# Kernel tuning notes

Measured on AMD Instinct MI355X. Metric: run time of the kernel, lower is better.

## Reference

```python
import jax, jax.numpy as jnp
import numpy as np

N = 10000      # nodes
E = 100000     # edges
D = 64         # node_out_feats
EH = 128       # edge_hidden_feats
NI = 74        # node_in_feats
EI = 12        # edge_in_feats
STEPS = 6


def _lin_init(key, fan_in, fan_out):
    s = 1.0 / np.sqrt(fan_in)
    kw, kb = jax.random.split(key)
    W = jax.random.uniform(kw, (fan_out, fan_in), minval=-s, maxval=s, dtype=jnp.float32)
    b = jax.random.uniform(kb, (fan_out,), minval=-s, maxval=s, dtype=jnp.float32)
    return W, b


def setup_inputs() -> dict:
    key = jax.random.key(0)
    ks = jax.random.split(key, 10)
    x = jax.random.normal(ks[0], (N, NI), dtype=jnp.float32)
    edge_index = jax.random.randint(ks[1], (2, E), 0, N, dtype=jnp.int64)
    edge_attr = jax.random.normal(ks[2], (E, EI), dtype=jnp.float32)
    W_proj, b_proj = _lin_init(ks[3], NI, D)
    W_e1, b_e1 = _lin_init(ks[4], EI, EH)
    W_e2, b_e2 = _lin_init(ks[5], EH, D * D)
    W_lin, b_lin = _lin_init(ks[6], D, D)
    s = 1.0 / np.sqrt(D)
    W_ih = jax.random.uniform(ks[7], (3 * D, D), minval=-s, maxval=s, dtype=jnp.float32)
    W_hh = jax.random.uniform(ks[8], (3 * D, D), minval=-s, maxval=s, dtype=jnp.float32)
    kb1, kb2 = jax.random.split(ks[9])
    b_ih = jax.random.uniform(kb1, (3 * D,), minval=-s, maxval=s, dtype=jnp.float32)
    b_hh = jax.random.uniform(kb2, (3 * D,), minval=-s, maxval=s, dtype=jnp.float32)
    return {"x": x, "edge_index": edge_index, "edge_attr": edge_attr,
            "W_proj": W_proj, "b_proj": b_proj,
            "W_e1": W_e1, "b_e1": b_e1, "W_e2": W_e2, "b_e2": b_e2,
            "W_lin": W_lin, "b_lin": b_lin,
            "W_ih": W_ih, "W_hh": W_hh, "b_ih": b_ih, "b_hh": b_hh}


def _gru_cell(x, h, W_ih, W_hh, b_ih, b_hh):
    # torch GRU gate layout: rows [r; z; n]
    gi = x @ W_ih.T + b_ih
    gh = h @ W_hh.T + b_hh
    i_r, i_z, i_n = jnp.split(gi, 3, axis=-1)
    h_r, h_z, h_n = jnp.split(gh, 3, axis=-1)
    r = jax.nn.sigmoid(i_r + h_r)
    z = jax.nn.sigmoid(i_z + h_z)
    n = jnp.tanh(i_n + r * h_n)
    return (1.0 - z) * n + z * h


def reference(x, edge_index, edge_attr, W_proj, b_proj, W_e1, b_e1, W_e2, b_e2,
              W_lin, b_lin, W_ih, W_hh, b_ih, b_hh):
    src = edge_index[0]
    dst = edge_index[1]
    n_nodes = x.shape[0]
    d = W_lin.shape[0]

    # project_node_feats
    node_feats = jax.nn.relu(x @ W_proj.T + b_proj)          # [N, D]
    hidden = node_feats                                       # h0 (never updated, per source)

    # edge network (identical each step in original; compute once)
    eh = jax.nn.relu(edge_attr @ W_e1.T + b_e1)               # [E, EH]
    A = (eh @ W_e2.T + b_e2).reshape(-1, d, d)                # [E, D, D]

    cnt = jax.ops.segment_sum(jnp.ones(src.shape, x.dtype), dst, num_segments=n_nodes)
    cnt = jnp.maximum(cnt, 1.0)[:, None]                      # mean divisor, 0-deg -> keep 0

    for _ in range(STEPS):
        xp = node_feats @ W_lin.T + b_lin                     # lin_node, [N, D]
        msg = jnp.einsum('ed,edf->ef', xp[src], A)            # per-edge bmm, [E, D]
        agg = jax.ops.segment_sum(msg, dst, num_segments=n_nodes) / cnt  # scatter-mean
        nf = jax.nn.relu(agg)
        node_feats = _gru_cell(nf, hidden, W_ih, W_hh, b_ih, b_hh)
    return node_feats
```

## Files before the change

kernel.cpp:

```cpp
#include <hip/hip_runtime.h>
#include <hip/hip_bf16.h>

#define NN 10000
#define NE 100000
#define DD 64
#define EH_ 128
#define NI_ 74
#define EI_ 12
#define NSTEPS 6
#define PADN 10240
#define GCAP 16384
#define EPB 64

#define RZ_OFF 0
#define NI_OFF 16384
#define NH_OFF 20480
#define WL_OFF 24576
#define BE_OFF 28672
#define G_TOT  32768

typedef short bf16x8 __attribute__((ext_vector_type(8)));
typedef float f32x4 __attribute__((ext_vector_type(4)));

static __device__ __forceinline__ unsigned short f2b(float f) {
    unsigned int u = __float_as_uint(f);
    u += 0x7fffu + ((u >> 16) & 1u);
    return (unsigned short)(u >> 16);
}

__global__ void k_zero(float* p, int n) {
    int i = blockIdx.x * blockDim.x + threadIdx.x;
    if (i < n) p[i] = 0.f;
}

__global__ void k_zero2(float* a, float* b, int n) {
    int i = blockIdx.x * blockDim.x + threadIdx.x;
    if (i < n) { a[i] = 0.f; b[i] = 0.f; }
}

__global__ void k_proj(const float* __restrict__ x, const float* __restrict__ Wp,
                       const float* __restrict__ bp, float* __restrict__ nf,
                       float* __restrict__ hid, unsigned short* __restrict__ hidb) {
    int w = (blockIdx.x * blockDim.x + threadIdx.x) >> 6;
    int lane = threadIdx.x & 63;
    if (w >= PADN) return;
    if (w >= NN) { hidb[(size_t)w * DD + lane] = 0; return; }
    const float* xr = x + (size_t)w * NI_;
    float x0 = xr[lane];
    float x1 = (lane < NI_ - 64) ? xr[64 + lane] : 0.f;
    float acc = bp[lane];
    const float* wr = Wp + (size_t)lane * NI_;
    #pragma unroll
    for (int i = 0; i < 64; i++) acc += __shfl(x0, i, 64) * wr[i];
    #pragma unroll
    for (int i = 0; i < NI_ - 64; i++) acc += __shfl(x1, i, 64) * wr[64 + i];
    acc = fmaxf(acc, 0.f);
    nf[(size_t)w * DD + lane] = acc;
    hid[(size_t)w * DD + lane] = acc;
    hidb[(size_t)w * DD + lane] = f2b(acc);
}

__global__ void k_degs(const int* __restrict__ srcv, const int* __restrict__ dstv,
                       int* __restrict__ hist, int* __restrict__ histd) {
    int e = blockIdx.x * blockDim.x + threadIdx.x;
    if (e < NE) {
        atomicAdd(&hist[srcv[e]], 1);
        atomicAdd(&histd[dstv[e]], 1);
    }
}

__global__ void k_scangrp(const int* __restrict__ hist, const int* __restrict__ histd,
                          int* __restrict__ rowptr, int* __restrict__ cursor,
                          int* __restrict__ g_src, int* __restrict__ g_base,
                          int* __restrict__ g_cnt, int* __restrict__ d_ng,
                          int* __restrict__ rowptrd, int* __restrict__ cursord) {
    __shared__ int part[1024];
    int t = threadIdx.x;
    const int PER = (NN + 1023) / 1024;
    int b0 = t * PER;
    int sum = 0;
    for (int i = 0; i < PER; i++) { int b = b0 + i; if (b < NN) sum += hist[b]; }
    part[t] = sum;
    __syncthreads();
    for (int off = 1; off < 1024; off <<= 1) {
        int v = (t >= off) ? part[t - off] : 0;
        __syncthreads();
        part[t] += v;
        __syncthreads();
    }
    int run = (t > 0) ? part[t - 1] : 0;
    for (int i = 0; i <= PER; i++) {
        int b = b0 + i;
        if (b <= NN) {
            rowptr[b] = run;
            if (b < NN) cursor[b] = run;
        }
        if (b < NN && i < PER) run += hist[b];
        if (i == PER) break;
    }
    __syncthreads();
    int cg = 0;
    for (int i = 0; i < PER; i++) {
        int b = b0 + i;
        if (b < NN) cg += (hist[b] + 15) >> 4;
    }
    part[t] = cg;
    __syncthreads();
    for (int off = 1; off < 1024; off <<= 1) {
        int v = (t >= off) ? part[t - off] : 0;
        __syncthreads();
        part[t] += v;
        __syncthreads();
    }
    int grun = (t > 0) ? part[t - 1] : 0;
    for (int i = 0; i < PER; i++) {
        int b = b0 + i;
        if (b >= NN) break;
        int r0 = rowptr[b], r1 = rowptr[b + 1];
        for (int p = r0; p < r1; p += 16) {
            g_src[grun] = b;
            g_base[grun] = p;
            int c = r1 - p; if (c > 16) c = 16;
            g_cnt[grun] = c;
            grun++;
        }
    }
    if (t == 1023) *d_ng = grun;
    __syncthreads();
    int sumd = 0;
    for (int i = 0; i < PER; i++) { int b = b0 + i; if (b < NN) sumd += histd[b]; }
    part[t] = sumd;
    __syncthreads();
    for (int off = 1; off < 1024; off <<= 1) {
        int v = (t >= off) ? part[t - off] : 0;
        __syncthreads();
        part[t] += v;
        __syncthreads();
    }
    int rund = (t > 0) ? part[t - 1] : 0;
    for (int i = 0; i <= PER; i++) {
        int b = b0 + i;
        if (b <= NN) {
            rowptrd[b] = rund;
            if (b < NN) cursord[b] = rund;
        }
        if (b < NN && i < PER) rund += histd[b];
        if (i == PER) break;
    }
}

__global__ void k_scatter(const int* __restrict__ srcv, const int* __restrict__ dstv,
                          int* __restrict__ cursor, int* __restrict__ cursord,
                          int* __restrict__ perm, int* __restrict__ permd) {
    int e = blockIdx.x * blockDim.x + threadIdx.x;
    if (e >= NE) return;
    int s = srcv[e];
    int d = dstv[e];
    int pos = atomicAdd(&cursor[s], 1);
    perm[pos] = e;
    int posd = atomicAdd(&cursord[d], 1);
    permd[posd] = pos;
}

__global__ void k_eh_s(const float* __restrict__ ea, const float* __restrict__ W1,
                       const float* __restrict__ b1, const int* __restrict__ perm,
                       unsigned short* __restrict__ ehs) {
    __shared__ float s_W[EH_ * EI_];
    __shared__ float s_b[EH_];
    __shared__ float s_ea[EPB][EI_];
    __shared__ int s_perm[EPB];
    int t = threadIdx.x;
    int p0 = blockIdx.x * EPB;
    for (int i = t; i < EH_ * EI_; i += 256) s_W[i] = W1[i];
    if (t < EH_) s_b[t] = b1[t];
    if (t < EPB) s_perm[t] = (p0 + t < NE) ? perm[p0 + t] : 0;
    __syncthreads();
    for (int i = t; i < EPB * EI_; i += 256) {
        int pl = i / EI_, ii = i % EI_;
        s_ea[pl][ii] = (p0 + pl < NE) ? ea[(size_t)s_perm[pl] * EI_ + ii] : 0.f;
    }
    int le = t >> 7;
    int h = t & 127;
    float wrow[EI_];
    #pragma unroll
    for (int i = 0; i < EI_; i++) wrow[i] = s_W[h * EI_ + i];
    float bb = s_b[h];
    __syncthreads();
    for (int pl = le; pl < EPB; pl += 2) {
        int p = p0 + pl;
        if (p >= NE) break;
        float acc = bb;
        #pragma unroll
        for (int i = 0; i < EI_; i++) acc += s_ea[pl][i] * wrow[i];
        ehs[(size_t)p * EH_ + h] = f2b(fmaxf(acc, 0.f));
    }
}

__global__ void k_pA(const float* __restrict__ W2, unsigned short* __restrict__ Apk) {
    int idx = blockIdx.x * 256 + threadIdx.x;
    if (idx >= (1 << 19)) return;
    int j = idx & 7;
    int n = (idx >> 3) & 15;
    int g = (idx >> 7) & 3;
    int frag = (idx >> 9) & 1;
    int f = (idx >> 10) & 63;
    int hB = (idx >> 16) & 1;
    int ks = idx >> 17;
    int d = frag * 32 + g * 8 + j;
    int h = ks * 32 + hB * 16 + n;
    Apk[idx] = f2b(W2[((size_t)(d * 64 + f)) * EH_ + h]);
}

__global__ void k_pG(const float* __restrict__ Wih, const float* __restrict__ Whh,
                     const float* __restrict__ Wl, const float* __restrict__ be2,
                     unsigned short* __restrict__ Gpk) {
    int idx = blockIdx.x * 256 + threadIdx.x;
    if (idx >= G_TOT) return;
    int j = idx & 7, n = (idx >> 3) & 15, g = (idx >> 7) & 3;
    float v;
    if (idx < NI_OFF) {
        int rem = idx >> 9;
        int q = rem & 3, ct = rem >> 2;
        int c = ct * 16 + n, k = q * 32 + g * 8 + j;
        v = (k < 64) ? Wih[(size_t)c * 64 + k] : Whh[(size_t)c * 64 + (k - 64)];
    } else if (idx < NH_OFF) {
        int l = idx - NI_OFF; int rem = l >> 9;
        int q = rem & 1, ct = rem >> 1;
        int c = ct * 16 + n, k = q * 32 + g * 8 + j;
        v = Wih[(size_t)(128 + c) * 64 + k];
    } else if (idx < WL_OFF) {
        int l = idx - NH_OFF; int rem = l >> 9;
        int q = rem & 1, ct = rem >> 1;
        int c = ct * 16 + n, k = q * 32 + g * 8 + j;
        v = Whh[(size_t)(128 + c) * 64 + k];
    } else if (idx < BE_OFF) {
        int l = idx - WL_OFF; int rem = l >> 9;
        int q = rem & 1, ct = rem >> 1;
        int c = ct * 16 + n, k = q * 32 + g * 8 + j;
        v = Wl[(size_t)c * 64 + k];
    } else {
        int l = idx - BE_OFF; int rem = l >> 9;
        int q = rem & 1, ct = rem >> 1;
        int c = ct * 16 + n, k = q * 32 + g * 8 + j;
        v = be2[(size_t)k * 64 + c];
    }
    Gpk[idx] = f2b(v);
}

__global__ void k_tr64(const float* __restrict__ W, float* __restrict__ Wt) {
    int idx = blockIdx.x * 256 + threadIdx.x;
    if (idx >= 64 * 64) return;
    int r = idx >> 6, c = idx & 63;
    Wt[c * 64 + r] = W[idx];
}

__global__ void k_prep(const float* __restrict__ msg, const int* __restrict__ rowptrd,
                       const int* __restrict__ permd, unsigned short* __restrict__ nfvb) {
    int wid = (blockIdx.x * blockDim.x + threadIdx.x) >> 6;
    int lane = threadIdx.x & 63;
    int s0 = wid * 4;
    if (s0 >= PADN) return;
    #pragma unroll
    for (int i = 0; i < 4; i++) {
        int node = s0 + i;
        if (node >= PADN) break;
        if (node >= NN) { nfvb[(size_t)node * DD + lane] = 0; continue; }
        int r0 = rowptrd[node], r1 = rowptrd[node + 1];
        float acc = 0.f;
        for (int p = r0; p < r1; p++) {
            int sp = permd[p];
            acc += msg[(size_t)sp * DD + lane];
        }
        float c = fmaxf((float)(r1 - r0), 1.f);
        nfvb[(size_t)node * DD + lane] = f2b(fmaxf(acc / c, 0.f));
    }
}

__global__ void k_xp(const float* __restrict__ nf, const float* __restrict__ WlT,
                     const float* __restrict__ bl, const float* __restrict__ be2,
                     unsigned short* __restrict__ xpb, float* __restrict__ btp) {
    int wid = (blockIdx.x * blockDim.x + threadIdx.x) >> 6;
    int lane = threadIdx.x & 63;
    int s0 = wid * 4;
    if (s0 >= NN) return;
    int nv = (NN - s0 < 4) ? (NN - s0) : 4;
    float nvv[4], acc[4], bt[4];
    float blv = bl[lane];
    #pragma unroll
    for (int i = 0; i < 4; i++) {
        int s = s0 + (i < nv ? i : nv - 1);
        nvv[i] = nf[(size_t)s * DD + lane];
        acc[i] = blv;
        bt[i] = 0.f;
    }
    for (int d = 0; d < 64; d++) {
        float wv = WlT[d * 64 + lane];
        #pragma unroll
        for (int i = 0; i < 4; i++)
            acc[i] = fmaf(__shfl(nvv[i], d, 64), wv, acc[i]);
    }
    for (int d = 0; d < 64; d++) {
        float bv = be2[d * 64 + lane];
        #pragma unroll
        for (int i = 0; i < 4; i++)
            bt[i] = fmaf(__shfl(acc[i], d, 64), bv, bt[i]);
    }
    #pragma unroll
    for (int i = 0; i < 4; i++) {
        if (i < nv) {
            xpb[(size_t)(s0 + i) * DD + lane] = f2b(acc[i]);
            btp[(size_t)(s0 + i) * DD + lane] = bt[i];
        }
    }
}

__global__ __launch_bounds__(1024, 8) void k_fv(
        const unsigned short* __restrict__ xpb,
        const unsigned short* __restrict__ Apk,
        const int* __restrict__ g_src, const int* __restrict__ g_base,
        const int* __restrict__ g_cnt, const int* __restrict__ d_ng,
        const unsigned short* __restrict__ ehs,
        const float* __restrict__ btp, float* __restrict__ msg) {
    __shared__ unsigned char lds[65536];
    int ng = *d_ng;
    int nb = blockIdx.x * 16;
    if (nb >= ng) return;
    int tid = threadIdx.x;
    int w = tid >> 6, lane = tid & 63;
    int g = lane >> 4, n = lane & 15;

    int srcn = g_src[nb + n];
    const unsigned short* xr = xpb + (size_t)srcn * DD + g * 8;
    bf16x8 xb0 = *(const bf16x8*)xr;
    bf16x8 xb1 = *(const bf16x8*)(xr + 32);

    int gi = nb + w;
    int sq = g_src[gi], bq = g_base[gi], cq = g_cnt[gi];

    f32x4 acc[4];
    #pragma unroll
    for (int nt = 0; nt < 4; nt++) {
        f32x4 z = {0.f, 0.f, 0.f, 0.f};
        acc[nt] = z;
    }

    for (int ks = 0; ks < 4; ks++) {
        if (ks) __syncthreads();
        #pragma unroll
        for (int hB = 0; hB < 2; hB++) {
            int ho = hB * 2 + (g >> 1);
            int hq0 = (g & 1) * 4;
            int abase = (n << 12) | (ho << 4) | (hq0 << 1);
            const unsigned short* apks =
                Apk + (size_t)((ks * 2 + hB) * 64 + (w << 2)) * 1024 + g * 128 + n * 8;
            #pragma unroll
            for (int fi = 0; fi < 4; fi++) {
                int f = (w << 2) + fi;
                const unsigned short* ap = apks + fi * 1024;
                bf16x8 A0 = *(const bf16x8*)ap;
                bf16x8 A1 = *(const bf16x8*)(ap + 512);
                f32x4 d = {0.f, 0.f, 0.f, 0.f};
                d = __builtin_amdgcn_mfma_f32_16x16x32_bf16(A0, xb0, d, 0, 0, 0);
                d = __builtin_amdgcn_mfma_f32_16x16x32_bf16(A1, xb1, d, 0, 0, 0);
                unsigned int lo = (unsigned)f2b(d[0]) | ((unsigned)f2b(d[1]) << 16);
                unsigned int hi = (unsigned)f2b(d[2]) | ((unsigned)f2b(d[3]) << 16);
                int addr = abase | (f << 6);
                addr ^= ((n ^ f) & 7) << 4;
                *(unsigned long long*)(lds + addr) =
                    (unsigned long long)lo | ((unsigned long long)hi << 32);
            }
        }
        bf16x8 aeh = *(const bf16x8*)(ehs + (size_t)(bq + n) * EH_ + ks * 32 + g * 8);
        __syncthreads();
        bf16x8 Bf[4];
        #pragma unroll
        for (int nt = 0; nt < 4; nt++) {
            int f = nt * 16 + n;
            int addr = (w << 12) | (f << 6) | (g << 4);
            addr ^= ((w ^ f) & 7) << 4;
            Bf[nt] = *(const bf16x8*)(lds + addr);
        }
        #pragma unroll
        for (int nt = 0; nt < 4; nt++)
            acc[nt] = __builtin_amdgcn_mfma_f32_16x16x32_bf16(aeh, Bf[nt], acc[nt], 0, 0, 0);
    }
    if (cq == 0) return;
    #pragma unroll
    for (int nt = 0; nt < 4; nt++) {
        float btv = btp[(size_t)sq * DD + nt * 16 + n];
        #pragma unroll
        for (int rg = 0; rg < 4; rg++) {
            int m = g * 4 + rg;
            if (m < cq)
                msg[(size_t)(bq + m) * DD + nt * 16 + n] = acc[nt][rg] + btv;
        }
    }
}

__global__ void k_gx(const unsigned short* __restrict__ nfvb,
                     const unsigned short* __restrict__ hidb,
                     const float* __restrict__ hid,
                     const unsigned short* __restrict__ Gpk,
                     const float* __restrict__ bih, const float* __restrict__ bhh,
                     const float* __restrict__ bl,
                     float* __restrict__ out_nf, unsigned short* __restrict__ xpb,
                     float* __restrict__ btp, int doXp) {
    __shared__ unsigned short s_nf[64 * 64];
    __shared__ unsigned short s_xp[64 * 64];
    int tid = threadIdx.x;
    int w = tid >> 6, lane = tid & 63;
    int g = lane >> 4, n = lane & 15;
    int nb = blockIdx.x * 64;
    int jj = w * 16 + n;

    bf16x8 Br[4], Bz[4], Bi[2], Bh[2], Bw[2], Be[2];
    #pragma unroll
    for (int q = 0; q < 4; q++) {
        Br[q] = *(const bf16x8*)(Gpk + RZ_OFF + (size_t)(((w) * 4 + q) * 4 + g) * 128 + n * 8);
        Bz[q] = *(const bf16x8*)(Gpk + RZ_OFF + (size_t)(((w + 4) * 4 + q) * 4 + g) * 128 + n * 8);
    }
    #pragma unroll
    for (int q = 0; q < 2; q++) {
        Bi[q] = *(const bf16x8*)(Gpk + NI_OFF + (size_t)((w * 2 + q) * 4 + g) * 128 + n * 8);
        Bh[q] = *(const bf16x8*)(Gpk + NH_OFF + (size_t)((w * 2 + q) * 4 + g) * 128 + n * 8);
        Bw[q] = *(const bf16x8*)(Gpk + WL_OFF + (size_t)((w * 2 + q) * 4 + g) * 128 + n * 8);
        Be[q] = *(const bf16x8*)(Gpk + BE_OFF + (size_t)((w * 2 + q) * 4 + g) * 128 + n * 8);
    }
    float br_ = bih[jj] + bhh[jj];
    float bz_ = bih[64 + jj] + bhh[64 + jj];
    float bi_ = bih[128 + jj];
    float bh_ = bhh[128 + jj];
    float blv = bl[jj];

    #pragma unroll
    for (int mt = 0; mt < 4; mt++) {
        int arow = nb + mt * 16 + n;
        const unsigned short* na = nfvb + (size_t)arow * DD + g * 8;
        const unsigned short* ha = hidb + (size_t)arow * DD + g * 8;
        bf16x8 A0 = *(const bf16x8*)na, A1 = *(const bf16x8*)(na + 32);
        bf16x8 H0 = *(const bf16x8*)ha, H1 = *(const bf16x8*)(ha + 32);
        f32x4 aR = {0.f, 0.f, 0.f, 0.f}, aZ = aR, aI = aR, aH = aR;
        aR = __builtin_amdgcn_mfma_f32_16x16x32_bf16(A0, Br[0], aR, 0, 0, 0);
        aR = __builtin_amdgcn_mfma_f32_16x16x32_bf16(A1, Br[1], aR, 0, 0, 0);
        aR = __builtin_amdgcn_mfma_f32_16x16x32_bf16(H0, Br[2], aR, 0, 0, 0);
        aR = __builtin_amdgcn_mfma_f32_16x16x32_bf16(H1, Br[3], aR, 0, 0, 0);
        aZ = __builtin_amdgcn_mfma_f32_16x16x32_bf16(A0, Bz[0], aZ, 0, 0, 0);
        aZ = __builtin_amdgcn_mfma_f32_16x16x32_bf16(A1, Bz[1], aZ, 0, 0, 0);
        aZ = __builtin_amdgcn_mfma_f32_16x16x32_bf16(H0, Bz[2], aZ, 0, 0, 0);
        aZ = __builtin_amdgcn_mfma_f32_16x16x32_bf16(H1, Bz[3], aZ, 0, 0, 0);
        aI = __builtin_amdgcn_mfma_f32_16x16x32_bf16(A0, Bi[0], aI, 0, 0, 0);
        aI = __builtin_amdgcn_mfma_f32_16x16x32_bf16(A1, Bi[1], aI, 0, 0, 0);
        aH = __builtin_amdgcn_mfma_f32_16x16x32_bf16(H0, Bh[0], aH, 0, 0, 0);
        aH = __builtin_amdgcn_mfma_f32_16x16x32_bf16(H1, Bh[1], aH, 0, 0, 0);
        #pragma unroll
        for (int rg = 0; rg < 4; rg++) {
            int row = mt * 16 + g * 4 + rg;
            int node = nb + row;
            float r = 1.f / (1.f + __expf(-(aR[rg] + br_)));
            float z = 1.f / (1.f + __expf(-(aZ[rg] + bz_)));
            float nn2 = tanhf(aI[rg] + bi_ + r * (aH[rg] + bh_));
            float hv = (node < NN) ? hid[(size_t)node * DD + jj] : 0.f;
            float nf_ = (1.f - z) * nn2 + z * hv;
            if (node < NN) out_nf[(size_t)node * DD + jj] = nf_;
            int ba = (row * 128 + jj * 2) ^ ((row & 7) << 4);
            s_nf[ba >> 1] = f2b(nf_);
        }
    }
    if (!doXp) return;
    __syncthreads();
    #pragma unroll
    for (int mt = 0; mt < 4; mt++) {
        int row = mt * 16 + n;
        int sw = (row & 7) << 4;
        bf16x8 X0 = *(const bf16x8*)((const unsigned char*)s_nf + ((row * 128 + g * 16) ^ sw));
        bf16x8 X1 = *(const bf16x8*)((const unsigned char*)s_nf + ((row * 128 + 64 + g * 16) ^ sw));
        f32x4 aX = {0.f, 0.f, 0.f, 0.f};
        aX = __builtin_amdgcn_mfma_f32_16x16x32_bf16(X0, Bw[0], aX, 0, 0, 0);
        aX = __builtin_amdgcn_mfma_f32_16x16x32_bf16(X1, Bw[1], aX, 0, 0, 0);
        #pragma unroll
        for (int rg = 0; rg < 4; rg++) {
            int row2 = mt * 16 + g * 4 + rg;
            int ba = (row2 * 128 + jj * 2) ^ ((row2 & 7) << 4);
            s_xp[ba >> 1] = f2b(aX[rg] + blv);
        }
    }
    __syncthreads();
    {
        int row = w * 16 + n;
        int sw = (row & 7) << 4;
        #pragma unroll
        for (int h2 = 0; h2 < 2; h2++) {
            int byteo = (row * 128 + (h2 * 4 + g) * 16) ^ sw;
            bf16x8 v = *(const bf16x8*)((const unsigned char*)s_xp + byteo);
            *(bf16x8*)(xpb + (size_t)(nb + row) * DD + (h2 * 4 + g) * 8) = v;
        }
    }
    #pragma unroll
    for (int mt = 0; mt < 4; mt++) {
        int row = mt * 16 + n;
        int sw = (row & 7) << 4;
        bf16x8 X0 = *(const bf16x8*)((const unsigned char*)s_xp + ((row * 128 + g * 16) ^ sw));
        bf16x8 X1 = *(const bf16x8*)((const unsigned char*)s_xp + ((row * 128 + 64 + g * 16) ^ sw));
        f32x4 aB = {0.f, 0.f, 0.f, 0.f};
        aB = __builtin_amdgcn_mfma_f32_16x16x32_bf16(X0, Be[0], aB, 0, 0, 0);
        aB = __builtin_amdgcn_mfma_f32_16x16x32_bf16(X1, Be[1], aB, 0, 0, 0);
        #pragma unroll
        for (int rg = 0; rg < 4; rg++) {
            int node = nb + mt * 16 + g * 4 + rg;
            if (node < NN) btp[(size_t)node * DD + jj] = aB[rg];
        }
    }
}

extern "C" void kernel_launch(void* const* d_in, const int* in_sizes, int n_in,
                              void* d_out, int out_size, void* d_ws, size_t ws_size,
                              hipStream_t stream) {
    const float* x   = (const float*)d_in[0];
    const int*   ei  = (const int*)d_in[1];
    const float* ea  = (const float*)d_in[2];
    const float* Wp  = (const float*)d_in[3];
    const float* bp  = (const float*)d_in[4];
    const float* W1  = (const float*)d_in[5];
    const float* b1  = (const float*)d_in[6];
    const float* W2  = (const float*)d_in[7];
    const float* b2  = (const float*)d_in[8];
    const float* Wl  = (const float*)d_in[9];
    const float* bl  = (const float*)d_in[10];
    const float* Wih = (const float*)d_in[11];
    const float* Whh = (const float*)d_in[12];
    const float* bih = (const float*)d_in[13];
    const float* bhh = (const float*)d_in[14];
    const int* srcv = ei;
    const int* dstv = ei + NE;

    float* p = (float*)d_ws;
    size_t off = 0;
    auto alloc = [&](size_t n) { n = (n + 3) & ~(size_t)3; float* q = p + off; off += n; return q; };
    float* nf   = alloc((size_t)NN * DD);
    float* hid  = alloc((size_t)NN * DD);
    float* btp  = alloc((size_t)NN * DD);
    unsigned short* ehs = (unsigned short*)alloc((size_t)(NE + 16) * EH_ / 2);
    float* WlT  = alloc(64 * 64);
    int* hist   = (int*)alloc(NN);
    int* histd  = (int*)alloc(NN);
    int* rowptr = (int*)alloc(NN + 1);
    int* cursor = (int*)alloc(NN);
    int* rowptrd = (int*)alloc(NN + 1);
    int* cursord = (int*)alloc(NN);
    int* perm   = (int*)alloc(NE);
    int* permd  = (int*)alloc(NE);
    int* g_src  = (int*)alloc(GCAP);
    int* g_base = (int*)alloc(GCAP);
    int* g_cnt  = (int*)alloc(GCAP);
    int* d_ng   = (int*)alloc(4);
    unsigned short* Apk  = (unsigned short*)alloc((size_t)(1 << 19) / 2);
    unsigned short* Gpk  = (unsigned short*)alloc((size_t)G_TOT / 2);
    unsigned short* xpb  = (unsigned short*)alloc((size_t)PADN * DD / 2);
    unsigned short* nfvb = (unsigned short*)alloc((size_t)PADN * DD / 2);
    unsigned short* hidb = (unsigned short*)alloc((size_t)PADN * DD / 2);
    float* msg = alloc((size_t)NE * DD);

    k_zero<<<(2 * NN + 255) / 256, 256, 0, stream>>>((float*)hist, 2 * NN);
    k_zero<<<(3 * GCAP + 255) / 256, 256, 0, stream>>>((float*)g_src, 3 * GCAP);
    k_proj<<<(PADN + 3) / 4, 256, 0, stream>>>(x, Wp, bp, nf, hid, hidb);
    k_pA<<<(1 << 19) / 256, 256, 0, stream>>>(W2, Apk);
    k_pG<<<(G_TOT + 255) / 256, 256, 0, stream>>>(Wih, Whh, Wl, b2, Gpk);
    k_tr64<<<16, 256, 0, stream>>>(Wl, WlT);
    k_degs<<<(NE + 255) / 256, 256, 0, stream>>>(srcv, dstv, hist, histd);
    k_scangrp<<<1, 1024, 0, stream>>>(hist, histd, rowptr, cursor,
                                      g_src, g_base, g_cnt, d_ng, rowptrd, cursord);
    k_scatter<<<(NE + 255) / 256, 256, 0, stream>>>(srcv, dstv, cursor, cursord,
                                                    perm, permd);
    k_eh_s<<<(NE + EPB - 1) / EPB, 256, 0, stream>>>(ea, W1, b1, perm, ehs);

    const int nw_quarter = (NN + 3) / 4;
    const int gx_blocks = (NN + 63) / 64;
    const int prep_blocks = (PADN / 4 + 3) / 4;
    k_xp<<<(nw_quarter + 3) / 4, 256, 0, stream>>>(nf, WlT, bl, b2, xpb, btp);
    for (int s = 0; s < NSTEPS; s++) {
        k_fv<<<GCAP / 16, 1024, 0, stream>>>(xpb, Apk, g_src, g_base, g_cnt, d_ng,
                                             ehs, btp, msg);
        k_prep<<<prep_blocks, 256, 0, stream>>>(msg, rowptrd, permd, nfvb);
        float* dest = (s == NSTEPS - 1) ? (float*)d_out : nf;
        k_gx<<<gx_blocks, 256, 0, stream>>>(nfvb, hidb, hid, Gpk, bih, bhh, bl,
                                            dest, xpb, btp,
                                            (s < NSTEPS - 1) ? 1 : 0);
    }
}
```

Before: 676.4 us.

## Write edge messages in destination order so aggregation reads contiguously

The message kernel now scatters each edge's message row directly to its destination-sorted position, using a source-to-destination position map built during the edge scatter. The aggregation kernel then sums contiguous message rows per node without indirection, and runs one node per wavefront instead of four. This moves random access from the reduction reads to the message writes. It also removes an unused zero kernel.

```diff
diff --git a/kernel.cpp b/kernel.cpp
--- a/kernel.cpp
+++ b/kernel.cpp
@@ -31,11 +31,6 @@
 __global__ void k_zero(float* p, int n) {
     int i = blockIdx.x * blockDim.x + threadIdx.x;
     if (i < n) p[i] = 0.f;
-}
-
-__global__ void k_zero2(float* a, float* b, int n) {
-    int i = blockIdx.x * blockDim.x + threadIdx.x;
-    if (i < n) { a[i] = 0.f; b[i] = 0.f; }
 }
 
 __global__ void k_proj(const float* __restrict__ x, const float* __restrict__ Wp,
@@ -151,7 +146,7 @@
 
 __global__ void k_scatter(const int* __restrict__ srcv, const int* __restrict__ dstv,
                           int* __restrict__ cursor, int* __restrict__ cursord,
-                          int* __restrict__ perm, int* __restrict__ permd) {
+                          int* __restrict__ perm, int* __restrict__ s2d) {
     int e = blockIdx.x * blockDim.x + threadIdx.x;
     if (e >= NE) return;
     int s = srcv[e];
@@ -159,7 +154,7 @@
     int pos = atomicAdd(&cursor[s], 1);
     perm[pos] = e;
     int posd = atomicAdd(&cursord[d], 1);
-    permd[posd] = pos;
+    s2d[pos] = posd;
 }
 
 __global__ void k_eh_s(const float* __restrict__ ea, const float* __restrict__ W1,
@@ -255,25 +250,17 @@
 }
 
 __global__ void k_prep(const float* __restrict__ msg, const int* __restrict__ rowptrd,
-                       const int* __restrict__ permd, unsigned short* __restrict__ nfvb) {
-    int wid = (blockIdx.x * blockDim.x + threadIdx.x) >> 6;
+                       unsigned short* __restrict__ nfvb) {
+    int node = (blockIdx.x * blockDim.x + threadIdx.x) >> 6;
     int lane = threadIdx.x & 63;
-    int s0 = wid * 4;
-    if (s0 >= PADN) return;
-    #pragma unroll
-    for (int i = 0; i < 4; i++) {
-        int node = s0 + i;
-        if (node >= PADN) break;
-        if (node >= NN) { nfvb[(size_t)node * DD + lane] = 0; continue; }
-        int r0 = rowptrd[node], r1 = rowptrd[node + 1];
-        float acc = 0.f;
-        for (int p = r0; p < r1; p++) {
-            int sp = permd[p];
-            acc += msg[(size_t)sp * DD + lane];
-        }
-        float c = fmaxf((float)(r1 - r0), 1.f);
-        nfvb[(size_t)node * DD + lane] = f2b(fmaxf(acc / c, 0.f));
-    }
+    if (node >= PADN) return;
+    if (node >= NN) { nfvb[(size_t)node * DD + lane] = 0; return; }
+    int r0 = rowptrd[node], r1 = rowptrd[node + 1];
+    float acc = 0.f;
+    for (int p = r0; p < r1; p++)
+        acc += msg[(size_t)p * DD + lane];
+    float c = fmaxf((float)(r1 - r0), 1.f);
+    nfvb[(size_t)node * DD + lane] = f2b(fmaxf(acc / c, 0.f));
 }
 
 __global__ void k_xp(const float* __restrict__ nf, const float* __restrict__ WlT,
@@ -319,7 +306,7 @@
         const unsigned short* __restrict__ Apk,
         const int* __restrict__ g_src, const int* __restrict__ g_base,
         const int* __restrict__ g_cnt, const int* __restrict__ d_ng,
-        const unsigned short* __restrict__ ehs,
+        const unsigned short* __restrict__ ehs, const int* __restrict__ s2d,
         const float* __restrict__ btp, float* __restrict__ msg) {
     __shared__ unsigned char lds[65536];
     int ng = *d_ng;
@@ -385,14 +372,19 @@
             acc[nt] = __builtin_amdgcn_mfma_f32_16x16x32_bf16(aeh, Bf[nt], acc[nt], 0, 0, 0);
     }
     if (cq == 0) return;
+    int dpr[4];
+    #pragma unroll
+    for (int rg = 0; rg < 4; rg++) {
+        int m = g * 4 + rg;
+        dpr[rg] = (m < cq) ? s2d[bq + m] : -1;
+    }
     #pragma unroll
     for (int nt = 0; nt < 4; nt++) {
         float btv = btp[(size_t)sq * DD + nt * 16 + n];
         #pragma unroll
         for (int rg = 0; rg < 4; rg++) {
-            int m = g * 4 + rg;
-            if (m < cq)
-                msg[(size_t)(bq + m) * DD + nt * 16 + n] = acc[nt][rg] + btv;
+            if (dpr[rg] >= 0)
+                msg[(size_t)dpr[rg] * DD + nt * 16 + n] = acc[nt][rg] + btv;
         }
     }
 }
@@ -548,7 +540,7 @@
     int* rowptrd = (int*)alloc(NN + 1);
     int* cursord = (int*)alloc(NN);
     int* perm   = (int*)alloc(NE);
-    int* permd  = (int*)alloc(NE);
+    int* s2d    = (int*)alloc(NE);
     int* g_src  = (int*)alloc(GCAP);
     int* g_base = (int*)alloc(GCAP);
     int* g_cnt  = (int*)alloc(GCAP);
@@ -570,17 +562,17 @@
     k_scangrp<<<1, 1024, 0, stream>>>(hist, histd, rowptr, cursor,
                                       g_src, g_base, g_cnt, d_ng, rowptrd, cursord);
     k_scatter<<<(NE + 255) / 256, 256, 0, stream>>>(srcv, dstv, cursor, cursord,
-                                                    perm, permd);
+                                                    perm, s2d);
     k_eh_s<<<(NE + EPB - 1) / EPB, 256, 0, stream>>>(ea, W1, b1, perm, ehs);
 
     const int nw_quarter = (NN + 3) / 4;
     const int gx_blocks = (NN + 63) / 64;
-    const int prep_blocks = (PADN / 4 + 3) / 4;
+    const int prep_blocks = PADN / 4;
     k_xp<<<(nw_quarter + 3) / 4, 256, 0, stream>>>(nf, WlT, bl, b2, xpb, btp);
     for (int s = 0; s < NSTEPS; s++) {
         k_fv<<<GCAP / 16, 1024, 0, stream>>>(xpb, Apk, g_src, g_base, g_cnt, d_ng,
-                                             ehs, btp, msg);
-        k_prep<<<prep_blocks, 256, 0, stream>>>(msg, rowptrd, permd, nfvb);
+                                             ehs, s2d, btp, msg);
+        k_prep<<<prep_blocks, 256, 0, stream>>>(msg, rowptrd, nfvb);
         float* dest = (s == NSTEPS - 1) ? (float*)d_out : nf;
         k_gx<<<gx_blocks, 256, 0, stream>>>(nfvb, hidb, hid, Gpk, bih, bhh, bl,
                                             dest, xpb, btp,
```

New measurement: 580.3 us. -14.2%, faster.
